# Optimization experiments

Hardware: AMD Instinct MI355X
Metric: run time of the kernel (lower is better)

Reference implementation:

```python
import jax, jax.numpy as jnp
from jax import lax
import numpy as np

F = 64          # filters
KH = KW = 3     # kernel size
STRIDE = 16     # input conv stride


def setup_inputs() -> dict:
    key = jax.random.key(0)
    k1, k2, k3, k4 = jax.random.split(key, 4)
    B, T, H, W, C = 16, 8, 256, 256, 3
    x = jax.random.normal(k1, (B, T, H, W, C), dtype=jnp.float32)
    # Keras ConvLSTM2D fuses the 4 gates (i, f, c, o) along output channels.
    Wx = jax.random.normal(k2, (KH, KW, C, 4 * F), dtype=jnp.float32) * 0.05
    Wh = jax.random.normal(k3, (KH, KW, F, 4 * F), dtype=jnp.float32) * 0.05
    b = jax.random.normal(k4, (4 * F,), dtype=jnp.float32) * 0.05
    return {"x": x, "Wx": Wx, "Wh": Wh, "b": b}


def _conv(inp, kern, strides):
    return lax.conv_general_dilated(
        inp, kern, window_strides=strides, padding="SAME",
        dimension_numbers=("NHWC", "HWIO", "NHWC"))


def _hard_sigmoid(z):
    # Keras ConvLSTM2D default recurrent_activation
    return jnp.clip(0.2 * z + 0.5, 0.0, 1.0)


def reference(x, Wx, Wh, b):
    B, T, H, W, C = x.shape
    # Strided input conv for all timesteps at once: (B*T,H,W,C) -> (B*T,Ho,Wo,4F)
    xc = _conv(x.reshape(B * T, H, W, C), Wx, (STRIDE, STRIDE))
    Ho, Wo = xc.shape[1], xc.shape[2]
    xc = (xc + b).reshape(B, T, Ho, Wo, 4 * F).transpose(1, 0, 2, 3, 4)  # (T,B,Ho,Wo,4F)

    def step(carry, xt):
        h, c = carry
        z = xt + _conv(h, Wh, (1, 1))          # (B,Ho,Wo,4F)
        zi, zf, zg, zo = jnp.split(z, 4, axis=-1)
        i = _hard_sigmoid(zi)
        f = _hard_sigmoid(zf)
        c = f * c + i * zg                     # activation=None -> linear g
        o = _hard_sigmoid(zo)
        h = o * c                              # activation=None -> linear cell output
        return (h, c), None

    h0 = jnp.zeros((B, Ho, Wo, F), dtype=x.dtype)
    c0 = jnp.zeros((B, Ho, Wo, F), dtype=x.dtype)
    (h, _), _ = lax.scan(step, (h0, c0), xc)
    return h  # return_sequences=False -> last hidden state (B,Ho,Wo,F)
```

## Files before the change

kernel.cpp:

```cpp
#include <hip/hip_runtime.h>

#define NB   16
#define NT   8
#define HIN  256
#define CIN  3
#define NF   64
#define OC   256
#define HO   16
#define WOUT 16

typedef short short8 __attribute__((ext_vector_type(8)));
typedef float f32x4 __attribute__((ext_vector_type(4)));

__device__ __forceinline__ unsigned short f2bf(float x) {
  union { float f; unsigned int u; } v; v.f = x;
  unsigned int r = v.u + 0x7fffu + ((v.u >> 16) & 1u);
  return (unsigned short)(r >> 16);
}
__device__ __forceinline__ float bf2f(unsigned short b) {
  union { unsigned int u; float f; } v; v.u = ((unsigned int)b) << 16;
  return v.f;
}

__global__ __launch_bounds__(256) void input_conv(
    const float* __restrict__ x, const float* __restrict__ Wx,
    const float* __restrict__ bias, float* __restrict__ xc)
{
  const int ho = blockIdx.x;
  const int bt = blockIdx.y;
  const int oc = threadIdx.x;

  __shared__ float patch[432];
  for (int idx = threadIdx.x; idx < 432; idx += 256) {
    int r = idx / 144, rem = idx % 144;
    int wo = rem / 9, k = rem % 9;
    int kw = k / 3, c = k % 3;
    patch[idx] = x[(((size_t)bt * HIN + (ho * 16 + r)) * HIN + (wo * 16 + kw)) * CIN + c];
  }
  float w[27];
#pragma unroll
  for (int k = 0; k < 27; ++k) w[k] = Wx[(size_t)k * OC + oc];
  __syncthreads();

  const float bv = bias[oc];
  const int n = (oc & 63) * 4 + (oc >> 6);
  for (int wo = 0; wo < 16; ++wo) {
    float acc = bv;
#pragma unroll
    for (int kh = 0; kh < 3; ++kh)
#pragma unroll
      for (int k9 = 0; k9 < 9; ++k9)
        acc = fmaf(patch[(kh * 16 + wo) * 9 + k9], w[kh * 9 + k9], acc);
    xc[(((size_t)bt * HO + ho) * WOUT + wo) * OC + n] = acc;
  }
}

__global__ __launch_bounds__(256) void conv_weights(
    const float* __restrict__ Wh, unsigned short* __restrict__ Bp)
{
  int idx = blockIdx.x * 256 + threadIdx.x;
  int c   = idx >> 14;
  int rem = idx & 16383;
  int n   = rem >> 6;
  int k   = rem & 63;
  int pass = c / 9, tap = c % 9;
  int kh = tap / 3, kw = tap % 3;
  int oc = (n & 3) * 64 + (n >> 2);
  float w = Wh[(size_t)((kh * 3 + kw) * 64 + k) * OC + oc];
  unsigned short hi = f2bf(w);
  Bp[idx] = (pass == 1) ? f2bf(w - bf2f(hi)) : hi;
}

__global__ __launch_bounds__(256) void lstm_step_mfma(
    const float* __restrict__ xc, const unsigned short* __restrict__ Bp,
    const unsigned short* __restrict__ h_hi_in, const unsigned short* __restrict__ h_lo_in,
    unsigned short* __restrict__ h_hi_out, unsigned short* __restrict__ h_lo_out,
    float* __restrict__ c_st, float* __restrict__ out,
    int t, int first, int last)
{
  const int mb  = blockIdx.x;
  const int nb  = blockIdx.y;
  const int b   = mb >> 2;
  const int ho0 = (mb & 3) * 4;
  const int n0  = nb * 64;
  const int tid = threadIdx.x;

  __shared__ __align__(16) union SM {
    unsigned short ab[2][2][64][72];
    float z[64][80];
  } sm;

  f32x4 acc[2][2];
#pragma unroll
  for (int i = 0; i < 2; ++i)
#pragma unroll
    for (int j = 0; j < 2; ++j) acc[i][j] = (f32x4)(0.0f);

  const int row = tid >> 2;
  const int q   = tid & 3;

  float4 ra0, ra1, rb0, rb1;
  const float4 zero4 = make_float4(0.f, 0.f, 0.f, 0.f);

  auto load_chunk = [&](int c) {
    int pass = c / 9, tap = c % 9;
    int kh = tap / 3, kw = tap % 3;
    const unsigned short* hsrc = (pass < 2) ? h_hi_in : h_lo_in;
    int y = ho0 + (row >> 4) + kh - 1;
    int xx = (row & 15) + kw - 1;
    ra0 = zero4; ra1 = zero4;
    if ((unsigned)y < 16u && (unsigned)xx < 16u) {
      const float4* p = (const float4*)(hsrc + (((size_t)b * 256 + y * 16 + xx) * 64 + q * 16));
      ra0 = p[0]; ra1 = p[1];
    }
    const float4* pb = (const float4*)(Bp + (((size_t)c * 256 + n0 + row) * 64 + q * 16));
    rb0 = pb[0]; rb1 = pb[1];
  };
  auto write_chunk = [&](int buf) {
    *(float4*)&sm.ab[buf][0][row][q * 16]     = ra0;
    *(float4*)&sm.ab[buf][0][row][q * 16 + 8] = ra1;
    *(float4*)&sm.ab[buf][1][row][q * 16]     = rb0;
    *(float4*)&sm.ab[buf][1][row][q * 16 + 8] = rb1;
  };

  const int wv   = tid >> 6;
  const int lane = tid & 63;
  const int moff = (wv & 1) * 32;
  const int noff = (wv >> 1) * 32;
  const int r16  = lane & 15;
  const int kg   = lane >> 4;

  auto compute_chunk = [&](int buf) {
#pragma unroll
    for (int kh2 = 0; kh2 < 2; ++kh2) {
      int ko = kh2 * 32 + kg * 8;
      short8 a0 = *(const short8*)&sm.ab[buf][0][moff + r16][ko];
      short8 a1 = *(const short8*)&sm.ab[buf][0][moff + 16 + r16][ko];
      short8 b0 = *(const short8*)&sm.ab[buf][1][noff + r16][ko];
      short8 b1 = *(const short8*)&sm.ab[buf][1][noff + 16 + r16][ko];
      acc[0][0] = __builtin_amdgcn_mfma_f32_16x16x32_bf16(a0, b0, acc[0][0], 0, 0, 0);
      acc[0][1] = __builtin_amdgcn_mfma_f32_16x16x32_bf16(a0, b1, acc[0][1], 0, 0, 0);
      acc[1][0] = __builtin_amdgcn_mfma_f32_16x16x32_bf16(a1, b0, acc[1][0], 0, 0, 0);
      acc[1][1] = __builtin_amdgcn_mfma_f32_16x16x32_bf16(a1, b1, acc[1][1], 0, 0, 0);
    }
  };

  if (!first) {
    load_chunk(0);
    for (int c = 0; c < 27; ++c) {
      write_chunk(c & 1);
      __syncthreads();
      if (c < 26) load_chunk(c + 1);
      compute_chunk(c & 1);
    }
  }
  __syncthreads();

#pragma unroll
  for (int mi = 0; mi < 2; ++mi)
#pragma unroll
    for (int ni = 0; ni < 2; ++ni)
#pragma unroll
      for (int i = 0; i < 4; ++i)
        sm.z[moff + mi * 16 + kg * 4 + i][noff + ni * 16 + r16] = acc[mi][ni][i];
  __syncthreads();

  const int fl   = tid & 15;
  const int mgrp = (tid >> 4) * 4;
  const int fglob = nb * 16 + fl;
  const float* xcb = xc + ((size_t)(b * NT + t) * 256) * 256;
#pragma unroll
  for (int mi = 0; mi < 4; ++mi) {
    int m   = mgrp + mi;
    int pos = ho0 * 16 + m;
    float4 zq = *(const float4*)&sm.z[m][fl * 4];
    float4 xq = *(const float4*)&xcb[(size_t)pos * OC + n0 + fl * 4];
    float zi = zq.x + xq.x, zf = zq.y + xq.y, zg = zq.z + xq.z, zo = zq.w + xq.w;
    float ig = fminf(fmaxf(fmaf(zi, 0.2f, 0.5f), 0.f), 1.f);
    float fg = fminf(fmaxf(fmaf(zf, 0.2f, 0.5f), 0.f), 1.f);
    float og = fminf(fmaxf(fmaf(zo, 0.2f, 0.5f), 0.f), 1.f);
    size_t cidx = ((size_t)b * 256 + pos) * NF + fglob;
    float cold = first ? 0.f : c_st[cidx];
    float cnew = fmaf(fg, cold, ig * zg);
    c_st[cidx] = cnew;
    float h = og * cnew;
    unsigned short hh = f2bf(h);
    h_hi_out[cidx] = hh;
    h_lo_out[cidx] = f2bf(h - bf2f(hh));
    if (last) out[cidx] = h;
  }
}

extern "C" void kernel_launch(void* const* d_in, const int* in_sizes, int n_in,
                              void* d_out, int out_size, void* d_ws, size_t ws_size,
                              hipStream_t stream) {
  const float* x    = (const float*)d_in[0];
  const float* Wx   = (const float*)d_in[1];
  const float* Wh   = (const float*)d_in[2];
  const float* bias = (const float*)d_in[3];
  float* out = (float*)d_out;

  char* ws = (char*)d_ws;
  float*          xc  = (float*)ws;
  unsigned short* Bp  = (unsigned short*)(ws + 33554432);
  unsigned short* h_hi[2] = { (unsigned short*)(ws + 34439168),
                              (unsigned short*)(ws + 34963456) };
  unsigned short* h_lo[2] = { (unsigned short*)(ws + 35487744),
                              (unsigned short*)(ws + 36012032) };
  float*          cbuf = (float*)(ws + 36536320);

  input_conv<<<dim3(HO, NB * NT), 256, 0, stream>>>(x, Wx, bias, xc);
  conv_weights<<<1728, 256, 0, stream>>>(Wh, Bp);

  for (int t = 0; t < NT; ++t) {
    int in  = t & 1;
    int outb = (t + 1) & 1;
    lstm_step_mfma<<<dim3(64, 4), 256, 0, stream>>>(
        xc, Bp, h_hi[in], h_lo[in], h_hi[outb], h_lo[outb],
        cbuf, out, t, t == 0, t == NT - 1);
  }
}
```

Measured before the change: 267.3 us.

## Restructure recurrent conv as split-K 32x32 MFMA with register-direct fragment loads

Rewrites the per-timestep LSTM kernel so each of 8 waves handles a slice of the K dimension (taps x precision passes x channel quarters) with 32x32x16 bf16 MFMAs. A and B fragments are loaded straight from global memory in pre-swizzled layouts, and the wave partials are reduced in shared memory. The hidden state is stored in a channel-blocked layout and the weight-prep kernel emits MFMA-fragment-ordered weights, so the LDS staging and per-chunk barriers go away. The grid grows to 512 blocks of 512 threads for more parallelism, at the cost of an LDS reduction over 8 partials and uncoalesced scattered 2-byte h stores.

```diff
diff --git a/kernel.cpp b/kernel.cpp
--- a/kernel.cpp
+++ b/kernel.cpp
@@ -10,7 +10,8 @@
 #define WOUT 16
 
 typedef short short8 __attribute__((ext_vector_type(8)));
-typedef float f32x4 __attribute__((ext_vector_type(4)));
+typedef float f32x4  __attribute__((ext_vector_type(4)));
+typedef float f32x16 __attribute__((ext_vector_type(16)));
 
 __device__ __forceinline__ unsigned short f2bf(float x) {
   union { float f; unsigned int u; } v; v.f = x;
@@ -56,139 +57,119 @@
 }
 
 __global__ __launch_bounds__(256) void conv_weights(
-    const float* __restrict__ Wh, unsigned short* __restrict__ Bp)
+    const float* __restrict__ Wh, unsigned short* __restrict__ Bp2)
 {
-  int idx = blockIdx.x * 256 + threadIdx.x;
-  int c   = idx >> 14;
-  int rem = idx & 16383;
-  int n   = rem >> 6;
-  int k   = rem & 63;
-  int pass = c / 9, tap = c % 9;
-  int kh = tap / 3, kw = tap % 3;
-  int oc = (n & 3) * 64 + (n >> 2);
-  float w = Wh[(size_t)((kh * 3 + kw) * 64 + k) * OC + oc];
-  unsigned short hi = f2bf(w);
-  Bp[idx] = (pass == 1) ? f2bf(w - bf2f(hi)) : hi;
-}
-
-__global__ __launch_bounds__(256) void lstm_step_mfma(
-    const float* __restrict__ xc, const unsigned short* __restrict__ Bp,
+  int thr = blockIdx.x * 256 + threadIdx.x;
+  int lane = thr & 63;
+  int q    = (thr >> 6) & 3;
+  int nfg  = (thr >> 8) & 7;
+  int c    = thr >> 11;
+  int pass = (c >= 18) ? 2 : (c >= 9 ? 1 : 0);
+  int tap  = c - pass * 9;
+  int n    = nfg * 32 + (lane & 31);
+  int kb   = q * 16 + (lane >> 5) * 8;
+  int oc   = (n & 3) * 64 + (n >> 2);
+  short8 v;
+#pragma unroll
+  for (int j = 0; j < 8; ++j) {
+    float w = Wh[(size_t)(tap * 64 + kb + j) * OC + oc];
+    unsigned short hi = f2bf(w);
+    v[j] = (short)((pass == 1) ? f2bf(w - bf2f(hi)) : hi);
+  }
+  *(short8*)(Bp2 + (size_t)thr * 8) = v;
+}
+
+__global__ __launch_bounds__(512, 4) void lstm_step_mfma(
+    const float* __restrict__ xc, const unsigned short* __restrict__ Bp2,
     const unsigned short* __restrict__ h_hi_in, const unsigned short* __restrict__ h_lo_in,
     unsigned short* __restrict__ h_hi_out, unsigned short* __restrict__ h_lo_out,
     float* __restrict__ c_st, float* __restrict__ out,
     int t, int first, int last)
 {
-  const int mb  = blockIdx.x;
-  const int nb  = blockIdx.y;
-  const int b   = mb >> 2;
-  const int ho0 = (mb & 3) * 4;
-  const int n0  = nb * 64;
-  const int tid = threadIdx.x;
-
-  __shared__ __align__(16) union SM {
-    unsigned short ab[2][2][64][72];
-    float z[64][80];
-  } sm;
-
-  f32x4 acc[2][2];
-#pragma unroll
-  for (int i = 0; i < 2; ++i)
-#pragma unroll
-    for (int j = 0; j < 2; ++j) acc[i][j] = (f32x4)(0.0f);
-
-  const int row = tid >> 2;
-  const int q   = tid & 3;
-
-  float4 ra0, ra1, rb0, rb1;
-  const float4 zero4 = make_float4(0.f, 0.f, 0.f, 0.f);
-
-  auto load_chunk = [&](int c) {
-    int pass = c / 9, tap = c % 9;
-    int kh = tap / 3, kw = tap % 3;
-    const unsigned short* hsrc = (pass < 2) ? h_hi_in : h_lo_in;
-    int y = ho0 + (row >> 4) + kh - 1;
-    int xx = (row & 15) + kw - 1;
-    ra0 = zero4; ra1 = zero4;
-    if ((unsigned)y < 16u && (unsigned)xx < 16u) {
-      const float4* p = (const float4*)(hsrc + (((size_t)b * 256 + y * 16 + xx) * 64 + q * 16));
-      ra0 = p[0]; ra1 = p[1];
+  const int mb   = blockIdx.x;
+  const int nb   = blockIdx.y;
+  const int b    = mb >> 3;
+  const int pos0 = (mb & 7) * 32;
+  const int tid  = threadIdx.x;
+  const int w    = tid >> 6;
+  const int lane = tid & 63;
+  const int col  = lane & 31;
+  const int kh2  = lane >> 5;
+
+  __shared__ float zpart[8][32][64];
+
+  if (!first) {
+    f32x16 acc0 = (f32x16)(0.0f), acc1 = (f32x16)(0.0f);
+
+    const int pos = pos0 + col;
+    const int hoq = pos >> 4, woq = pos & 15;
+
+    auto unit_load = [&](int u, short8& a, short8& b0, short8& b1) {
+      int c = u >> 2, q = u & 3;
+      int pass = (c >= 18) ? 2 : (c >= 9 ? 1 : 0);
+      int tap  = c - pass * 9;
+      int kh = ((tap * 11) >> 5) - 1;
+      int kw = (tap - (kh + 1) * 3) - 1;
+      int y = hoq + kh, xx = woq + kw;
+      a = (short8)0;
+      if ((unsigned)y < 16u && (unsigned)xx < 16u) {
+        const unsigned short* hsrc = (pass < 2) ? h_hi_in : h_lo_in;
+        int kq = q * 2 + kh2;
+        a = *(const short8*)(hsrc + ((((b * 8 + kq) * 256) + (y * 16 + xx)) * 8));
+      }
+      const unsigned short* bp = Bp2 + (size_t)((((c * 8 + nb * 2) * 4 + q) * 64 + lane) * 8);
+      b0 = *(const short8*)bp;
+      b1 = *(const short8*)(bp + 2048);
+    };
+
+    short8 a, b0, b1, a2, b02, b12;
+    int u = w;
+    unit_load(u, a, b0, b1);
+    for (; u + 8 < 108; u += 8) {
+      unit_load(u + 8, a2, b02, b12);
+      acc0 = __builtin_amdgcn_mfma_f32_32x32x16_bf16(a, b0, acc0, 0, 0, 0);
+      acc1 = __builtin_amdgcn_mfma_f32_32x32x16_bf16(a, b1, acc1, 0, 0, 0);
+      a = a2; b0 = b02; b1 = b12;
     }
-    const float4* pb = (const float4*)(Bp + (((size_t)c * 256 + n0 + row) * 64 + q * 16));
-    rb0 = pb[0]; rb1 = pb[1];
-  };
-  auto write_chunk = [&](int buf) {
-    *(float4*)&sm.ab[buf][0][row][q * 16]     = ra0;
-    *(float4*)&sm.ab[buf][0][row][q * 16 + 8] = ra1;
-    *(float4*)&sm.ab[buf][1][row][q * 16]     = rb0;
-    *(float4*)&sm.ab[buf][1][row][q * 16 + 8] = rb1;
-  };
-
-  const int wv   = tid >> 6;
-  const int lane = tid & 63;
-  const int moff = (wv & 1) * 32;
-  const int noff = (wv >> 1) * 32;
-  const int r16  = lane & 15;
-  const int kg   = lane >> 4;
-
-  auto compute_chunk = [&](int buf) {
-#pragma unroll
-    for (int kh2 = 0; kh2 < 2; ++kh2) {
-      int ko = kh2 * 32 + kg * 8;
-      short8 a0 = *(const short8*)&sm.ab[buf][0][moff + r16][ko];
-      short8 a1 = *(const short8*)&sm.ab[buf][0][moff + 16 + r16][ko];
-      short8 b0 = *(const short8*)&sm.ab[buf][1][noff + r16][ko];
-      short8 b1 = *(const short8*)&sm.ab[buf][1][noff + 16 + r16][ko];
-      acc[0][0] = __builtin_amdgcn_mfma_f32_16x16x32_bf16(a0, b0, acc[0][0], 0, 0, 0);
-      acc[0][1] = __builtin_amdgcn_mfma_f32_16x16x32_bf16(a0, b1, acc[0][1], 0, 0, 0);
-      acc[1][0] = __builtin_amdgcn_mfma_f32_16x16x32_bf16(a1, b0, acc[1][0], 0, 0, 0);
-      acc[1][1] = __builtin_amdgcn_mfma_f32_16x16x32_bf16(a1, b1, acc[1][1], 0, 0, 0);
+    acc0 = __builtin_amdgcn_mfma_f32_32x32x16_bf16(a, b0, acc0, 0, 0, 0);
+    acc1 = __builtin_amdgcn_mfma_f32_32x32x16_bf16(a, b1, acc1, 0, 0, 0);
+
+#pragma unroll
+    for (int r = 0; r < 16; ++r) {
+      int row = (r & 3) + 8 * (r >> 2) + 4 * kh2;
+      zpart[w][row][col]      = acc0[r];
+      zpart[w][row][32 + col] = acc1[r];
     }
-  };
-
+  }
+  __syncthreads();
+
+  const int m  = tid >> 4;
+  const int fl = tid & 15;
+  const int pos = pos0 + m;
+  float4 z = make_float4(0.f, 0.f, 0.f, 0.f);
   if (!first) {
-    load_chunk(0);
-    for (int c = 0; c < 27; ++c) {
-      write_chunk(c & 1);
-      __syncthreads();
-      if (c < 26) load_chunk(c + 1);
-      compute_chunk(c & 1);
+#pragma unroll
+    for (int ww = 0; ww < 8; ++ww) {
+      float4 p = *(const float4*)&zpart[ww][m][fl * 4];
+      z.x += p.x; z.y += p.y; z.z += p.z; z.w += p.w;
     }
   }
-  __syncthreads();
-
-#pragma unroll
-  for (int mi = 0; mi < 2; ++mi)
-#pragma unroll
-    for (int ni = 0; ni < 2; ++ni)
-#pragma unroll
-      for (int i = 0; i < 4; ++i)
-        sm.z[moff + mi * 16 + kg * 4 + i][noff + ni * 16 + r16] = acc[mi][ni][i];
-  __syncthreads();
-
-  const int fl   = tid & 15;
-  const int mgrp = (tid >> 4) * 4;
-  const int fglob = nb * 16 + fl;
-  const float* xcb = xc + ((size_t)(b * NT + t) * 256) * 256;
-#pragma unroll
-  for (int mi = 0; mi < 4; ++mi) {
-    int m   = mgrp + mi;
-    int pos = ho0 * 16 + m;
-    float4 zq = *(const float4*)&sm.z[m][fl * 4];
-    float4 xq = *(const float4*)&xcb[(size_t)pos * OC + n0 + fl * 4];
-    float zi = zq.x + xq.x, zf = zq.y + xq.y, zg = zq.z + xq.z, zo = zq.w + xq.w;
-    float ig = fminf(fmaxf(fmaf(zi, 0.2f, 0.5f), 0.f), 1.f);
-    float fg = fminf(fmaxf(fmaf(zf, 0.2f, 0.5f), 0.f), 1.f);
-    float og = fminf(fmaxf(fmaf(zo, 0.2f, 0.5f), 0.f), 1.f);
-    size_t cidx = ((size_t)b * 256 + pos) * NF + fglob;
-    float cold = first ? 0.f : c_st[cidx];
-    float cnew = fmaf(fg, cold, ig * zg);
-    c_st[cidx] = cnew;
-    float h = og * cnew;
-    unsigned short hh = f2bf(h);
-    h_hi_out[cidx] = hh;
-    h_lo_out[cidx] = f2bf(h - bf2f(hh));
-    if (last) out[cidx] = h;
-  }
+  const float4 xq = *(const float4*)&xc[(((size_t)(b * NT + t) * 256) + pos) * OC + nb * 64 + fl * 4];
+  float zi = z.x + xq.x, zf = z.y + xq.y, zg = z.z + xq.z, zo = z.w + xq.w;
+  float ig = fminf(fmaxf(fmaf(zi, 0.2f, 0.5f), 0.f), 1.f);
+  float fg = fminf(fmaxf(fmaf(zf, 0.2f, 0.5f), 0.f), 1.f);
+  float og = fminf(fmaxf(fmaf(zo, 0.2f, 0.5f), 0.f), 1.f);
+  const int f = nb * 16 + fl;
+  size_t cidx = ((size_t)b * 256 + pos) * NF + f;
+  float cold = first ? 0.f : c_st[cidx];
+  float cnew = fmaf(fg, cold, ig * zg);
+  c_st[cidx] = cnew;
+  float h = og * cnew;
+  unsigned short hh = f2bf(h);
+  size_t hidx = ((size_t)(b * 8 + (f >> 3)) * 256 + pos) * 8 + (f & 7);
+  h_hi_out[hidx] = hh;
+  h_lo_out[hidx] = f2bf(h - bf2f(hh));
+  if (last) out[cidx] = h;
 }
 
 extern "C" void kernel_launch(void* const* d_in, const int* in_sizes, int n_in,
@@ -202,7 +183,7 @@
 
   char* ws = (char*)d_ws;
   float*          xc  = (float*)ws;
-  unsigned short* Bp  = (unsigned short*)(ws + 33554432);
+  unsigned short* Bp2 = (unsigned short*)(ws + 33554432);
   unsigned short* h_hi[2] = { (unsigned short*)(ws + 34439168),
                               (unsigned short*)(ws + 34963456) };
   unsigned short* h_lo[2] = { (unsigned short*)(ws + 35487744),
@@ -210,13 +191,13 @@
   float*          cbuf = (float*)(ws + 36536320);
 
   input_conv<<<dim3(HO, NB * NT), 256, 0, stream>>>(x, Wx, bias, xc);
-  conv_weights<<<1728, 256, 0, stream>>>(Wh, Bp);
+  conv_weights<<<216, 256, 0, stream>>>(Wh, Bp2);
 
   for (int t = 0; t < NT; ++t) {
     int in  = t & 1;
-    int outb = (t + 1) & 1;
-    lstm_step_mfma<<<dim3(64, 4), 256, 0, stream>>>(
-        xc, Bp, h_hi[in], h_lo[in], h_hi[outb], h_lo[outb],
+    int ob  = (t + 1) & 1;
+    lstm_step_mfma<<<dim3(128, 4), 512, 0, stream>>>(
+        xc, Bp2, h_hi[in], h_lo[in], h_hi[ob], h_lo[ob],
         cbuf, out, t, t == 0, t == NT - 1);
   }
 }
```

Measured after the change: 218.6 us. 18.2% less time.
